# Optimization experiments

Hardware: AMD Instinct MI355X
Metric: run time of the kernel (lower is better)

## Reference

```python
import jax, jax.numpy as jnp
import numpy as np

B, N_NUC, N_UP, N_DOWN = 512, 16, 32, 32
N_ELEC = N_UP + N_DOWN            # 64 electrons
F = 8                             # edge feature dim (Gaussian RBF envelopes)
D = N_NUC * F                     # embedding_dim = 128 (positional electron embeddings)
L = 3                             # n_interactions
N_ATOM_TYPES = 4


def _rbf(diff):
    # diff: [..., 3] -> [..., F]; Gaussian RBF features of the interparticle distance
    d = jnp.sqrt(jnp.sum(diff * diff, axis=-1) + 1e-12)
    mu = jnp.linspace(0.0, 4.0, F, dtype=diff.dtype)
    return jnp.exp(-(d[..., None] - mu) ** 2)


def setup_inputs() -> dict:
    key = jax.random.key(0)
    ks = jax.random.split(key, 9)
    r = 2.0 * jax.random.normal(ks[0], (B, N_ELEC, 3), dtype=jnp.float32)
    R = 2.0 * jax.random.normal(ks[1], (B, N_NUC, 3), dtype=jnp.float32)
    atom_types = jax.random.randint(ks[2], (N_NUC,), 0, N_ATOM_TYPES)
    embed_table = 0.1 * jax.random.normal(ks[3], (N_ATOM_TYPES, D), dtype=jnp.float32)
    we_same = 0.1 * jax.random.normal(ks[4], (L, F, D), dtype=jnp.float32)
    we_anti = 0.1 * jax.random.normal(ks[5], (L, F, D), dtype=jnp.float32)
    we_ne = 0.1 * jax.random.normal(ks[6], (L, F, D), dtype=jnp.float32)
    w_up = 0.05 * jax.random.normal(ks[7], (L, 4 * D, D), dtype=jnp.float32)
    b_up = jnp.zeros((L, D), dtype=jnp.float32)
    return {
        'r': r, 'R': R, 'embed_table': embed_table,
        'we_same': we_same, 'we_anti': we_anti, 'we_ne': we_ne,
        'w_up': w_up, 'b_up': b_up, 'atom_types': atom_types,
    }


def reference(r, R, embed_table, we_same, we_anti, we_ne, w_up, b_up, atom_types):
    # --- molecular graph edge construction (pairwise differences + edge features) ---
    ee_feat = _rbf(r[:, :, None, :] - r[:, None, :, :])   # [B, e, e, F]
    ne_feat = _rbf(r[:, :, None, :] - R[:, None, :, :])   # [B, e, n, F]

    spin = jnp.arange(N_ELEC) >= N_UP
    eye = jnp.eye(N_ELEC, dtype=bool)
    same_m = ((spin[:, None] == spin[None, :]) & ~eye).astype(ee_feat.dtype)  # no self-interaction
    anti_m = (spin[:, None] != spin[None, :]).astype(ee_feat.dtype)
    feat_same = ee_feat * same_m[None, :, :, None]
    feat_anti = ee_feat * anti_m[None, :, :, None]

    # --- node factory: positional electron embeddings (dense scatter of ne features == reshape) ---
    x = ne_feat.reshape(ne_feat.shape[0], N_ELEC, N_NUC * F)  # [B, e, D]
    y = embed_table[atom_types]                               # [n, D] nuclei embeddings

    # --- message-passing layers ---
    for l in range(L):
        # messages = Linear(edge_feats) * sender embedding, summed over senders per receiver;
        # contract sender axis first to keep intermediates at [B, e, F, D]
        t_s = jnp.einsum('bijf,bjd->bifd', feat_same, x)
        z_s = jnp.einsum('bifd,fd->bid', t_s, we_same[l])
        t_a = jnp.einsum('bijf,bjd->bifd', feat_anti, x)
        z_a = jnp.einsum('bifd,fd->bid', t_a, we_anti[l])
        t_n = jnp.einsum('binf,nd->bifd', ne_feat, y)
        z_n = jnp.einsum('bifd,fd->bid', t_n, we_ne[l])
        upd = jnp.concatenate([x, z_s, z_a, z_n], axis=-1)    # [B, e, 4D]
        x = x + jnp.tanh(upd @ w_up[l] + b_up[l])
    return x  # final electron embeddings [B, N_ELEC, D]
```

## Files before the change

kernel.cpp:

```cpp
#include <hip/hip_runtime.h>


typedef unsigned short u16;
typedef unsigned int u32;
typedef __attribute__((ext_vector_type(8))) short short8;
typedef __attribute__((ext_vector_type(4))) float f32x4;
typedef __attribute__((ext_vector_type(4))) u32 u32x4;
typedef _Float16 h2 __attribute__((ext_vector_type(2)));

__device__ __forceinline__ u16 f2h(float f){ return __builtin_bit_cast(u16, (_Float16)f); }
__device__ __forceinline__ float h2f(u16 a){ return (float)__builtin_bit_cast(_Float16, a); }

__device__ __forceinline__ short8 rbf8(float dd){
  short8 a;
#pragma unroll
  for (int f = 0; f < 8; f++){
    float u = dd - (4.0f/7.0f)*(float)f;
    a[f] = (short)f2h(__expf(-u*u));
  }
  return a;
}

__global__ __launch_bounds__(256) void gnn_prep(
    const float* __restrict__ w_up, const float* __restrict__ we_ne,
    const float* __restrict__ embed, const int* __restrict__ atypes,
    u16* __restrict__ wsegs){
  __shared__ u16 lw[16384];
  const int blk = blockIdx.x;
  const int l = blk / 5, seg = blk % 5;
  const int tid = threadIdx.x;
  if (seg < 4){
    const float* src = w_up + (l*512 + seg*128)*128;
#pragma unroll
    for (int mm = 0; mm < 16; mm++){
      int idx = mm*1024 + tid*4;
      float4 v = *(const float4*)(src + idx);
      lw[idx+0] = f2h(v.x); lw[idx+1] = f2h(v.y);
      lw[idx+2] = f2h(v.z); lw[idx+3] = f2h(v.w);
    }
  } else {
#pragma unroll
    for (int mm = 0; mm < 16; mm++){
      int idx = mm*1024 + tid*4;
      int k = idx >> 7, dout = idx & 127;
      int n = k >> 3, f = k & 7;
      float4 ye = *(const float4*)(embed + atypes[n]*128 + dout);
      float4 wn = *(const float4*)(we_ne + (l*8 + f)*128 + dout);
      lw[idx+0] = f2h(ye.x*wn.x); lw[idx+1] = f2h(ye.y*wn.y);
      lw[idx+2] = f2h(ye.z*wn.z); lw[idx+3] = f2h(ye.w*wn.w);
    }
  }
  __syncthreads();
  u16* dst = wsegs + blk*16384;
  const int col = tid & 15, q = (tid >> 4) & 3;
#pragma unroll
  for (int m = 0; m < 8; m++){
    int slot = m*4 + (tid >> 6);
    int c = slot >> 3, nt = slot & 7;
    int kbase = c*32 + q*8;
    int dout = nt*16 + col;
    short8 vv;
#pragma unroll
    for (int jj = 0; jj < 8; jj++) vv[jj] = (short)lw[(kbase+jj)*128 + dout];
    *(short8*)(dst + m*2048 + tid*8) = vv;
  }
}

__global__ __launch_bounds__(256, 2) void gnn_main(
    const float* __restrict__ r_g, const float* __restrict__ R_g,
    const float* __restrict__ weS_g, const float* __restrict__ weA_g,
    const float* __restrict__ bup_g,
    const u16* __restrict__ wsegs,
    float* __restrict__ out)
{
  extern __shared__ __attribute__((aligned(16))) u16 lds[];
  u16* const xb  = lds;
  u16* const zst = lds + 8704;
  float* const rs = (float*)(lds + 17408);
  float* const Rs = rs + 256;

  const int tid  = threadIdx.x;
  const int lane = tid & 63;
  const int w    = tid >> 6;
  const int b    = blockIdx.x;
  const int col  = lane & 15;
  const int q    = lane >> 4;
  const int i0   = w * 16;
  const int sp   = w >> 1;
  const int mrow = i0 + col;
  const int loff = (q*16 + col) * 8;

  auto gemm_seg = [&](const u16* wseg_g, const u16* arows, f32x4* acc){
#pragma unroll
    for (int c = 0; c < 4; c++){
      short8 a = *(const short8*)(arows + mrow*136 + c*32 + (q<<3));
#pragma unroll
      for (int nt = 0; nt < 8; nt++){
        short8 bf = *(const short8*)(wseg_g + c*4096 + nt*512 + loff);
        acc[nt] = __builtin_amdgcn_mfma_f32_16x16x32_f16(a, bf, acc[nt], 0, 0, 0);
      }
    }
  };

  short8 aS[8], aA[8];
  float dN[4];
  {
    if (tid < 64){
#pragma unroll
      for (int k = 0; k < 3; k++) rs[tid*4+k] = r_g[(b*64+tid)*3 + k];
    } else if (tid < 80){
      int n = tid - 64;
#pragma unroll
      for (int k = 0; k < 3; k++) Rs[n*4+k] = R_g[(b*16+n)*3 + k];
    }
    __syncthreads();
    {
      float x0 = rs[mrow*4], x1 = rs[mrow*4+1], x2 = rs[mrow*4+2];
#pragma unroll
      for (int c = 0; c < 8; c++){
        int j = 32*sp + 4*c + q;
        float dx = x0-rs[j*4], dy = x1-rs[j*4+1], dz = x2-rs[j*4+2];
        float dd = sqrtf(dx*dx + dy*dy + dz*dz + 1e-12f);
        aS[c] = rbf8(dd);
        if (j == mrow) aS[c] = (short8)0;
        j = 32*(1-sp) + 4*c + q;
        dx = x0-rs[j*4]; dy = x1-rs[j*4+1]; dz = x2-rs[j*4+2];
        aA[c] = rbf8(sqrtf(dx*dx + dy*dy + dz*dz + 1e-12f));
      }
#pragma unroll
      for (int c = 0; c < 4; c++){
        int n = 4*c + q;
        float dx = x0-Rs[n*4], dy = x1-Rs[n*4+1], dz = x2-Rs[n*4+2];
        dN[c] = sqrtf(dx*dx + dy*dy + dz*dz + 1e-12f);
      }
    }
    {
      int i = tid >> 2, nb = (tid & 3)*4;
      float y0 = rs[i*4], y1 = rs[i*4+1], y2 = rs[i*4+2];
#pragma unroll
      for (int nn = 0; nn < 4; nn++){
        int n = nb + nn;
        float dx = y0-Rs[n*4], dy = y1-Rs[n*4+1], dz = y2-Rs[n*4+2];
        float dd = sqrtf(dx*dx + dy*dy + dz*dz + 1e-12f);
        *(short8*)&xb[i*136 + n*8] = rbf8(dd);
      }
    }
    __syncthreads();
  }

  f32x4 xr[8];
#pragma unroll
  for (int nt = 0; nt < 8; nt++)
#pragma unroll
    for (int rr = 0; rr < 4; rr++)
      xr[nt][rr] = h2f(xb[(i0 + q*4 + rr)*136 + nt*16 + col]);

  const f32x4 vzero = {0.f, 0.f, 0.f, 0.f};

#pragma unroll 1
  for (int l = 0; l < 3; l++){
    const u16* slab = wsegs + l*81920;

    f32x4 upd[8];
#pragma unroll
    for (int nt = 0; nt < 8; nt++) upd[nt] = vzero;

    auto zpass = [&](int pass){
      const float* weX = pass ? weA_g : weS_g;
      const int jb0 = pass ? 32*(1-sp) : 32*sp;
      const short8* aF = pass ? aA : aS;
      f32x4 zacc[8];
#pragma unroll
      for (int nt = 0; nt < 8; nt++) zacc[nt] = vzero;
#pragma unroll
      for (int nt = 0; nt < 8; nt++){
        h2 wp[4];
#pragma unroll
        for (int p = 0; p < 4; p++){
          h2 t;
          t[0] = (_Float16)weX[(l*8 + 2*p  )*128 + nt*16 + col];
          t[1] = (_Float16)weX[(l*8 + 2*p+1)*128 + nt*16 + col];
          wp[p] = t;
        }
        u16 xv[8];
#pragma unroll
        for (int c = 0; c < 8; c++) xv[c] = xb[(jb0 + 4*c + q)*136 + nt*16 + col];
#pragma unroll
        for (int c = 0; c < 8; c++){
          _Float16 xh = __builtin_bit_cast(_Float16, xv[c]);
          h2 xd; xd[0] = xh; xd[1] = xh;
          u32x4 bu;
#pragma unroll
          for (int p = 0; p < 4; p++)
            bu[p] = __builtin_bit_cast(u32, (h2)(xd * wp[p]));
          short8 bf = __builtin_bit_cast(short8, bu);
          zacc[nt] = __builtin_amdgcn_mfma_f32_16x16x32_f16(aF[c], bf, zacc[nt], 0, 0, 0);
        }
      }
#pragma unroll
      for (int nt = 0; nt < 8; nt++)
#pragma unroll
        for (int rr = 0; rr < 4; rr++)
          zst[(i0 + q*4 + rr)*136 + nt*16 + col] = f2h(zacc[nt][rr]);
    };

    zpass(0);
    gemm_seg(slab + 0*16384, xb,  upd);
    gemm_seg(slab + 1*16384, zst, upd);
    zpass(1);
    gemm_seg(slab + 2*16384, zst, upd);
    {
      const u16* yseg = slab + 4*16384;
      f32x4 zn[8];
#pragma unroll
      for (int nt = 0; nt < 8; nt++) zn[nt] = vzero;
#pragma unroll
      for (int c = 0; c < 4; c++){
        short8 a = rbf8(dN[c]);
#pragma unroll
        for (int nt = 0; nt < 8; nt++){
          short8 bf = *(const short8*)(yseg + c*4096 + nt*512 + loff);
          zn[nt] = __builtin_amdgcn_mfma_f32_16x16x32_f16(a, bf, zn[nt], 0, 0, 0);
        }
      }
#pragma unroll
      for (int nt = 0; nt < 8; nt++)
#pragma unroll
        for (int rr = 0; rr < 4; rr++)
          zst[(i0 + q*4 + rr)*136 + nt*16 + col] = f2h(zn[nt][rr]);
    }
    gemm_seg(slab + 3*16384, zst, upd);

    {
      float bupr[8];
#pragma unroll
      for (int nt = 0; nt < 8; nt++) bupr[nt] = bup_g[l*128 + nt*16 + col];
#pragma unroll
      for (int nt = 0; nt < 8; nt++){
#pragma unroll
        for (int rr = 0; rr < 4; rr++){
          float v = upd[nt][rr] + bupr[nt];
          float e = __expf(2.0f * v);
          float th = 1.0f - 2.0f * __builtin_amdgcn_rcpf(e + 1.0f);
          xr[nt][rr] += th;
        }
      }
    }
    if (l < 2){
#pragma unroll
      for (int nt = 0; nt < 8; nt++)
#pragma unroll
        for (int rr = 0; rr < 4; rr++)
          xb[(i0 + q*4 + rr)*136 + nt*16 + col] = f2h(xr[nt][rr]);
      __syncthreads();
    } else {
#pragma unroll
      for (int nt = 0; nt < 8; nt++)
#pragma unroll
        for (int rr = 0; rr < 4; rr++)
          out[(b*64 + i0 + q*4 + rr)*128 + nt*16 + col] = xr[nt][rr];
    }
  }
}

extern "C" void kernel_launch(void* const* d_in, const int* in_sizes, int n_in,
                              void* d_out, int out_size, void* d_ws, size_t ws_size,
                              hipStream_t stream){
  const float* r     = (const float*)d_in[0];
  const float* R     = (const float*)d_in[1];
  const float* embed = (const float*)d_in[2];
  const float* weS   = (const float*)d_in[3];
  const float* weA   = (const float*)d_in[4];
  const float* weN   = (const float*)d_in[5];
  const float* wup   = (const float*)d_in[6];
  const float* bup   = (const float*)d_in[7];
  const int* atyp    = (const int*)d_in[8];

  u16* wsegs = (u16*)d_ws;

  (void)hipFuncSetAttribute((const void*)gnn_main,
                            hipFuncAttributeMaxDynamicSharedMemorySize, 36096);
  gnn_prep<<<15, 256, 0, stream>>>(wup, weN, embed, atyp, wsegs);
  gnn_main<<<512, 256, 36096, stream>>>(r, R, weS, weA, bup, wsegs, (float*)d_out);
}
```

Measured before the change: 142.5 us.

## Recompute edge RBF fragments per pass and stage packed edge weights in LDS

```diff
diff --git a/kernel.cpp b/kernel.cpp
--- a/kernel.cpp
+++ b/kernel.cpp
@@ -74,10 +74,12 @@
     float* __restrict__ out)
 {
   extern __shared__ __attribute__((aligned(16))) u16 lds[];
-  u16* const xb  = lds;
-  u16* const zst = lds + 8704;
-  float* const rs = (float*)(lds + 17408);
+  u16* const xb   = lds;
+  u16* const zst1 = lds + 8704;
+  u16* const zst2 = lds + 17408;
+  float* const rs = (float*)(lds + 26112);
   float* const Rs = rs + 256;
+  u32* const weP  = (u32*)(lds + 26752);
 
   const int tid  = threadIdx.x;
   const int lane = tid & 63;
@@ -102,7 +104,7 @@
     }
   };
 
-  short8 aS[8], aA[8];
+  float px0, px1, px2;
   float dN[4];
   {
     if (tid < 64){
@@ -113,26 +115,23 @@
 #pragma unroll
       for (int k = 0; k < 3; k++) Rs[n*4+k] = R_g[(b*16+n)*3 + k];
     }
+#pragma unroll
+    for (int e0 = 0; e0 < 3072; e0 += 256){
+      int e = e0 + tid;
+      int d = e & 127, p = (e >> 7) & 3, ps = (e >> 9) & 1, ll = e >> 10;
+      const float* src = ps ? weA_g : weS_g;
+      h2 t;
+      t[0] = (_Float16)src[(ll*8 + 2*p  )*128 + d];
+      t[1] = (_Float16)src[(ll*8 + 2*p+1)*128 + d];
+      weP[((ll*2+ps)*4 + p)*128 + d] = __builtin_bit_cast(u32, t);
+    }
     __syncthreads();
-    {
-      float x0 = rs[mrow*4], x1 = rs[mrow*4+1], x2 = rs[mrow*4+2];
-#pragma unroll
-      for (int c = 0; c < 8; c++){
-        int j = 32*sp + 4*c + q;
-        float dx = x0-rs[j*4], dy = x1-rs[j*4+1], dz = x2-rs[j*4+2];
-        float dd = sqrtf(dx*dx + dy*dy + dz*dz + 1e-12f);
-        aS[c] = rbf8(dd);
-        if (j == mrow) aS[c] = (short8)0;
-        j = 32*(1-sp) + 4*c + q;
-        dx = x0-rs[j*4]; dy = x1-rs[j*4+1]; dz = x2-rs[j*4+2];
-        aA[c] = rbf8(sqrtf(dx*dx + dy*dy + dz*dz + 1e-12f));
-      }
-#pragma unroll
-      for (int c = 0; c < 4; c++){
-        int n = 4*c + q;
-        float dx = x0-Rs[n*4], dy = x1-Rs[n*4+1], dz = x2-Rs[n*4+2];
-        dN[c] = sqrtf(dx*dx + dy*dy + dz*dz + 1e-12f);
-      }
+    px0 = rs[mrow*4]; px1 = rs[mrow*4+1]; px2 = rs[mrow*4+2];
+#pragma unroll
+    for (int c = 0; c < 4; c++){
+      int n = 4*c + q;
+      float dx = px0-Rs[n*4], dy = px1-Rs[n*4+1], dz = px2-Rs[n*4+2];
+      dN[c] = sqrtf(dx*dx + dy*dy + dz*dz + 1e-12f);
     }
     {
       int i = tid >> 2, nb = (tid & 3)*4;
@@ -165,50 +164,50 @@
 #pragma unroll
     for (int nt = 0; nt < 8; nt++) upd[nt] = vzero;
 
-    auto zpass = [&](int pass){
-      const float* weX = pass ? weA_g : weS_g;
+    auto zpass = [&](int pass, u16* zdst){
       const int jb0 = pass ? 32*(1-sp) : 32*sp;
-      const short8* aF = pass ? aA : aS;
+      const u32* wbase = weP + ((l*2 + pass)*4)*128;
+      h2 wpA[8][4];
+#pragma unroll
+      for (int nt = 0; nt < 8; nt++)
+#pragma unroll
+        for (int p = 0; p < 4; p++)
+          wpA[nt][p] = __builtin_bit_cast(h2, wbase[p*128 + nt*16 + col]);
       f32x4 zacc[8];
 #pragma unroll
       for (int nt = 0; nt < 8; nt++) zacc[nt] = vzero;
 #pragma unroll
-      for (int nt = 0; nt < 8; nt++){
-        h2 wp[4];
-#pragma unroll
-        for (int p = 0; p < 4; p++){
-          h2 t;
-          t[0] = (_Float16)weX[(l*8 + 2*p  )*128 + nt*16 + col];
-          t[1] = (_Float16)weX[(l*8 + 2*p+1)*128 + nt*16 + col];
-          wp[p] = t;
-        }
-        u16 xv[8];
-#pragma unroll
-        for (int c = 0; c < 8; c++) xv[c] = xb[(jb0 + 4*c + q)*136 + nt*16 + col];
-#pragma unroll
-        for (int c = 0; c < 8; c++){
-          _Float16 xh = __builtin_bit_cast(_Float16, xv[c]);
+      for (int c = 0; c < 8; c++){
+        int j = jb0 + 4*c + q;
+        float dx = px0-rs[j*4], dy = px1-rs[j*4+1], dz = px2-rs[j*4+2];
+        float dd = sqrtf(dx*dx + dy*dy + dz*dz + 1e-12f);
+        short8 a = rbf8(dd);
+        if (pass == 0 && j == mrow) a = (short8)0;
+#pragma unroll
+        for (int nt = 0; nt < 8; nt++){
+          u16 xvv = xb[j*136 + nt*16 + col];
+          _Float16 xh = __builtin_bit_cast(_Float16, xvv);
           h2 xd; xd[0] = xh; xd[1] = xh;
           u32x4 bu;
 #pragma unroll
           for (int p = 0; p < 4; p++)
-            bu[p] = __builtin_bit_cast(u32, (h2)(xd * wp[p]));
+            bu[p] = __builtin_bit_cast(u32, (h2)(xd * wpA[nt][p]));
           short8 bf = __builtin_bit_cast(short8, bu);
-          zacc[nt] = __builtin_amdgcn_mfma_f32_16x16x32_f16(aF[c], bf, zacc[nt], 0, 0, 0);
+          zacc[nt] = __builtin_amdgcn_mfma_f32_16x16x32_f16(a, bf, zacc[nt], 0, 0, 0);
         }
       }
 #pragma unroll
       for (int nt = 0; nt < 8; nt++)
 #pragma unroll
         for (int rr = 0; rr < 4; rr++)
-          zst[(i0 + q*4 + rr)*136 + nt*16 + col] = f2h(zacc[nt][rr]);
+          zdst[(i0 + q*4 + rr)*136 + nt*16 + col] = f2h(zacc[nt][rr]);
     };
 
-    zpass(0);
-    gemm_seg(slab + 0*16384, xb,  upd);
-    gemm_seg(slab + 1*16384, zst, upd);
-    zpass(1);
-    gemm_seg(slab + 2*16384, zst, upd);
+    zpass(0, zst1);
+    zpass(1, zst2);
+
+    gemm_seg(slab + 0*16384, xb,   upd);
+    gemm_seg(slab + 1*16384, zst1, upd);
     {
       const u16* yseg = slab + 4*16384;
       f32x4 zn[8];
@@ -227,9 +226,10 @@
       for (int nt = 0; nt < 8; nt++)
 #pragma unroll
         for (int rr = 0; rr < 4; rr++)
-          zst[(i0 + q*4 + rr)*136 + nt*16 + col] = f2h(zn[nt][rr]);
-    }
-    gemm_seg(slab + 3*16384, zst, upd);
+          zst1[(i0 + q*4 + rr)*136 + nt*16 + col] = f2h(zn[nt][rr]);
+    }
+    gemm_seg(slab + 2*16384, zst2, upd);
+    gemm_seg(slab + 3*16384, zst1, upd);
 
     {
       float bupr[8];
@@ -279,7 +279,7 @@
   u16* wsegs = (u16*)d_ws;
 
   (void)hipFuncSetAttribute((const void*)gnn_main,
-                            hipFuncAttributeMaxDynamicSharedMemorySize, 36096);
+                            hipFuncAttributeMaxDynamicSharedMemorySize, 65792);
   gnn_prep<<<15, 256, 0, stream>>>(wup, weN, embed, atyp, wsegs);
-  gnn_main<<<512, 256, 36096, stream>>>(r, R, weS, weA, bup, wsegs, (float*)d_out);
-}
+  gnn_main<<<512, 256, 65792, stream>>>(r, R, weS, weA, bup, wsegs, (float*)d_out);
+}
```

Measured after the change: 146.2 us. +2.5%, slower.
